# Kernel optimization log

Measured on AMD Instinct MI355X. Metric: run time of the kernel, lower is better.

## Reference

```python
import jax, jax.numpy as jnp
import numpy as np
import math

D_MODEL = 512
NUM_HEADS = 8
MAX_LEN = 10000.0


def positional_encoding_2d(seq_len, d_model, H, W, dtype=jnp.float32):
    # position along height repeated across width, and vice versa
    pos_h = jnp.repeat(jnp.arange(H, dtype=dtype), W)  # [H*W]
    pos_w = jnp.tile(jnp.arange(W, dtype=dtype), H)    # [H*W]
    div_term = jnp.exp(jnp.arange(0, d_model, 2, dtype=dtype) * (-(math.log(MAX_LEN) / d_model)))
    div = div_term[: d_model // 4]  # [d_model//4]
    pe = jnp.zeros((seq_len, d_model), dtype=dtype)
    pe = pe.at[:, 0::4].set(jnp.sin(pos_h[:, None] * div))
    pe = pe.at[:, 1::4].set(jnp.cos(pos_h[:, None] * div))
    pe = pe.at[:, 2::4].set(jnp.sin(pos_w[:, None] * div))
    pe = pe.at[:, 3::4].set(jnp.cos(pos_w[:, None] * div))
    return pe


def setup_inputs() -> dict:
    key = jax.random.key(0)
    ks = jax.random.split(key, 6)
    B, C, H, W = 8, D_MODEL, 32, 32
    d = D_MODEL
    s = 1.0 / math.sqrt(d)
    x = jax.random.normal(ks[0], (B, C, H, W), dtype=jnp.float32)
    Wq = jax.random.normal(ks[1], (d, d), dtype=jnp.float32) * s
    Wk = jax.random.normal(ks[2], (d, d), dtype=jnp.float32) * s
    Wv = jax.random.normal(ks[3], (d, d), dtype=jnp.float32) * s
    Wo = jax.random.normal(ks[4], (d, d), dtype=jnp.float32) * s
    bo = jnp.zeros((d,), dtype=jnp.float32)
    gamma = jnp.ones((d,), dtype=jnp.float32)
    beta = jnp.zeros((d,), dtype=jnp.float32)
    return {"x": x, "Wq": Wq, "Wk": Wk, "Wv": Wv, "Wo": Wo, "bo": bo, "gamma": gamma, "beta": beta}


def reference(x, Wq, Wk, Wv, Wo, bo, gamma, beta):
    B, C, H, W = x.shape
    d_model = C
    nh = NUM_HEADS
    dk = d_model // nh
    seq = H * W

    # [B, C, H, W] -> [B, seq, d_model]
    x_seq = x.reshape(B, C, seq).transpose(0, 2, 1)
    pe = positional_encoding_2d(seq, d_model, H, W, dtype=x.dtype)
    x_seq = x_seq + pe[None]
    residual = x_seq

    # QKV projections (torch Linear: y = x @ W.T)
    q = (x_seq @ Wq.T).reshape(B, seq, nh, dk).transpose(0, 2, 1, 3)  # [B, nh, S, dk]
    k = (x_seq @ Wk.T).reshape(B, seq, nh, dk).transpose(0, 2, 1, 3)
    v = (x_seq @ Wv.T).reshape(B, seq, nh, dk).transpose(0, 2, 1, 3)

    scores = jnp.einsum("bhsd,bhtd->bhst", q, k) / math.sqrt(dk)  # [B, nh, S, S]
    weights = jax.nn.softmax(scores, axis=-1)
    # dropout is identity at inference
    attn = jnp.einsum("bhst,bhtd->bhsd", weights, v)  # [B, nh, S, dk]
    attn = attn.transpose(0, 2, 1, 3).reshape(B, seq, d_model)

    out = attn @ Wo.T + bo
    y = out + residual
    mean = jnp.mean(y, axis=-1, keepdims=True)
    var = jnp.var(y, axis=-1, keepdims=True)
    y = (y - mean) / jnp.sqrt(var + 1e-5) * gamma + beta

    return y.transpose(0, 2, 1).reshape(B, C, H, W)
```

## Files before the change

kernel.cpp:

```cpp
#include <hip/hip_runtime.h>
#include <hip/hip_bf16.h>
#include <math.h>

#define DEV static __device__ __forceinline__

typedef unsigned short u16;
typedef unsigned int u32;
typedef __attribute__((ext_vector_type(4))) float f32x4;
typedef __attribute__((ext_vector_type(16))) float f32x16;
typedef __attribute__((ext_vector_type(8))) __bf16 bf16x8;
typedef __attribute__((ext_vector_type(4))) u16 u16x4;
typedef __attribute__((ext_vector_type(4))) u32 u32x4;

DEV u16 f2bf(float f) {
  unsigned u = __float_as_uint(f);
  u += 0x7fffu + ((u >> 16) & 1u);
  return (u16)(u >> 16);
}
DEV float bf2f(u16 x) { return __uint_as_float((u32)x << 16); }

DEV float fexp2(float x) { return __builtin_amdgcn_exp2f(x); }
DEV float fsin_rev(float rev) { return __builtin_amdgcn_sinf(rev); }
DEV float fcos_rev(float rev) { return __builtin_amdgcn_cosf(rev); }

DEV u32 cvt_pk_bf16(float lo, float hi) {
  u32 r;
  asm("v_cvt_pk_bf16_f32 %0, %1, %2" : "=v"(r) : "v"(lo), "v"(hi));
  return r;
}

DEV void perm32swap(u32& a, u32& b) {
  asm("v_permlane32_swap_b32 %0, %1" : "+v"(a), "+v"(b));
}

DEV void gl2lds16(const void* g, void* l) {
  __builtin_amdgcn_global_load_lds(
      (const __attribute__((address_space(1))) void*)g,
      (__attribute__((address_space(3))) void*)l, 16, 0, 0);
}

template<int RPW>
DEV void stage_rows(const u16* __restrict__ g, int gstride, u16* lds, int wave, int lane) {
  const int r_in = lane >> 3, slot = lane & 7;
  const int base_row = wave * RPW;
#pragma unroll
  for (int i = 0; i < RPW / 8; ++i) {
    const int row = base_row + i * 8 + r_in;
    const int sslot = slot ^ (row & 7);
    gl2lds16(g + (size_t)row * gstride + sslot * 8,
             lds + (size_t)(base_row + i * 8) * 64);
  }
}

DEV bf16x8 frag_read(const u16* lds, int row, int kslot) {
  const int slot = kslot ^ (row & 7);
  return *(const bf16x8*)(lds + row * 64 + slot * 8);
}

DEV f32x4 mfma16(bf16x8 a, bf16x8 b, f32x4 c) {
  return __builtin_amdgcn_mfma_f32_16x16x32_bf16(a, b, c, 0, 0, 0);
}
DEV f32x16 mfma32(bf16x8 a, bf16x8 b, f32x16 c) {
  return __builtin_amdgcn_mfma_f32_32x32x16_bf16(a, b, c, 0, 0, 0);
}

__global__ __launch_bounds__(256) void prep_x(
    const float* __restrict__ x, u16* __restrict__ Xp,
    const float* __restrict__ w0, const float* __restrict__ w1,
    const float* __restrict__ w2, const float* __restrict__ w3,
    u16* __restrict__ Wpk) {
  const int t = threadIdx.x;
  if (blockIdx.z == 8) {
    const int flat = blockIdx.x + 32 * blockIdx.y;
    const int wsel = flat >> 7, bx = flat & 127;
    const float* src = (wsel == 0) ? w0 : (wsel == 1) ? w1 : (wsel == 2) ? w2 : w3;
    const int lane = t & 63, wave = t >> 6;
    const int c16 = bx >> 2;
    const int kchunk = (bx & 3) * 4 + wave;
    const int cl = lane & 15, ko = lane >> 4;
    const float* s = src + (size_t)(c16 * 16 + cl) * 512 + kchunk * 32 + ko * 8;
    const f32x4 a = *(const f32x4*)(s);
    const f32x4 b = *(const f32x4*)(s + 4);
    u16x4 lo, hi;
#pragma unroll
    for (int j = 0; j < 4; ++j) { lo[j] = f2bf(a[j]); hi[j] = f2bf(b[j]); }
    u16* d = Wpk + (size_t)wsel * 262144
                 + (size_t)(c16 * 16 + kchunk) * 512 + lane * 8;
    *(u16x4*)(d) = lo;
    *(u16x4*)(d + 4) = hi;
    return;
  }
  __shared__ float tile[32][33];
  const int b = blockIdx.z, c0 = blockIdx.y * 32, s0 = blockIdx.x * 32;
  const int cf = t >> 5, sf = t & 31;
#pragma unroll
  for (int i = 0; i < 4; ++i) {
    const int c = c0 + cf + i * 8;
    tile[cf + i * 8][sf] = x[((size_t)b * 512 + c) * 1024 + s0 + sf];
  }
  __syncthreads();
  const int cl = t & 31, sl = t >> 5;
  const int cg = c0 + cl;
  const int j = cg >> 2;
  const float dv = fexp2((float)j * -0.051905126482615f);
  const float dv_rev = dv * 0.15915494309189535f;
#pragma unroll
  for (int i = 0; i < 4; ++i) {
    const int s = s0 + sl + i * 8;
    const float pos = (cg & 2) ? (float)(s & 31) : (float)(s >> 5);
    float rev = pos * dv_rev;
    rev = rev - floorf(rev);
    const float pe = (cg & 1) ? fcos_rev(rev) : fsin_rev(rev);
    const float v = tile[cl][sl + i * 8] + pe;
    Xp[((size_t)b * 1024 + s) * 512 + cg] = f2bf(v);
  }
}

__global__ __launch_bounds__(256) void gemm_qkv(
    const u16* __restrict__ Xp, const u16* __restrict__ Wpk,
    u16* __restrict__ Qb, u16* __restrict__ Kb, u16* __restrict__ Vtb,
    float qscale) {
  __shared__ __align__(16) u16 smem[16896];
  const int t = threadIdx.x, lane = t & 63, wave = t >> 6;
  const int bn0 = blockIdx.x * 128, bm0 = blockIdx.y * 128;
  const int wr = wave >> 1, wc = wave & 1;
  const int colbase = bn0 + wc * 64;
  const int w = colbase >> 9;
  const int cb16 = (colbase & 511) >> 4;
  const u16* Bf = Wpk + (size_t)w * 262144;
  const u16* Ag = Xp + (size_t)bm0 * 512;
  f32x4 acc[4][4] = {};
  stage_rows<32>(Ag, 512, smem, wave, lane);
  __syncthreads();
  int cur = 0;
  for (int kt = 0; kt < 512; kt += 64) {
    if (kt < 448)
      stage_rows<32>(Ag + kt + 64, 512, smem + (cur ^ 1) * 8192, wave, lane);
    u16* Asc = smem + cur * 8192;
#pragma unroll
    for (int ks = 0; ks < 2; ++ks) {
      const int kc = (kt >> 5) + ks;
      bf16x8 af[4], bfr[4];
#pragma unroll
      for (int n = 0; n < 4; ++n)
        bfr[n] = *(const bf16x8*)(Bf + (size_t)((cb16 + n) * 16 + kc) * 512 + lane * 8);
#pragma unroll
      for (int m = 0; m < 4; ++m)
        af[m] = frag_read(Asc, wr * 64 + m * 16 + (lane & 15), ks * 4 + (lane >> 4));
#pragma unroll
      for (int m = 0; m < 4; ++m)
#pragma unroll
        for (int n = 0; n < 4; ++n)
          acc[m][n] = mfma16(af[m], bfr[n], acc[m][n]);
    }
    __syncthreads();
    cur ^= 1;
  }
  const int cl = lane & 15, rg = (lane >> 4) * 4;
  if (bn0 >= 1024) {
#pragma unroll
    for (int m = 0; m < 4; ++m)
#pragma unroll
      for (int n = 0; n < 4; ++n) {
        const int dvL = wc * 64 + n * 16 + cl;
        const int rowL0 = wr * 64 + m * 16 + rg;
        u16x4 pk;
#pragma unroll
        for (int r = 0; r < 4; ++r) pk[r] = f2bf(acc[m][n][r]);
        *(u16x4*)(smem + dvL * 132 + rowL0) = pk;
      }
    __syncthreads();
    const int dvg0 = bn0 - 1024;
#pragma unroll
    for (int i = 0; i < 16; ++i) {
      const int idx = i * 256 + t;
      const int dv = idx >> 5, ch = (idx & 31) * 4;
      const u16x4 v = *(const u16x4*)(smem + dv * 132 + ch);
      *(u16x4*)(Vtb + (size_t)(dvg0 + dv) * 8192 + bm0 + ch) = v;
    }
  } else {
    u16* dst = (bn0 >= 512) ? Kb : Qb;
    const float al = (bn0 >= 512) ? 1.0f : qscale;
    const int cb = (bn0 & 511) + wc * 64;
#pragma unroll
    for (int m = 0; m < 4; ++m)
#pragma unroll
      for (int n = 0; n < 4; ++n) {
        const int col = cb + n * 16 + cl;
#pragma unroll
        for (int r = 0; r < 4; ++r) {
          const int row = bm0 + wr * 64 + m * 16 + rg + r;
          dst[(size_t)row * 512 + col] = f2bf(acc[m][n][r] * al);
        }
      }
  }
}

__global__ __launch_bounds__(512) void gemm_ln(
    const u16* __restrict__ A, const u16* __restrict__ Wpk,
    const u16* __restrict__ residb, const float* __restrict__ bias,
    const float* __restrict__ gamma, const float* __restrict__ beta,
    float* __restrict__ out) {
  __shared__ __align__(16) u16 smem[35200];
  __shared__ float redsum[8][32], redsq[8][32], srow[32][2];
  const int t = threadIdx.x, lane = t & 63, wave = t >> 6;
  const int m0 = blockIdx.x * 32;
  const int b = m0 >> 10, s0 = m0 & 1023;
  u16* As = smem;
  const u16* Bf = Wpk + (size_t)3 * 262144;
  const u16* Ag = A + (size_t)m0 * 512;
  f32x4 acc[2][4] = {};
  for (int kt = 0; kt < 512; kt += 64) {
    __syncthreads();
    if (wave < 4) stage_rows<8>(Ag + kt, 512, As, wave, lane);
    __syncthreads();
#pragma unroll
    for (int ks = 0; ks < 2; ++ks) {
      const int kc = (kt >> 5) + ks;
      bf16x8 af[2], bfr[4];
#pragma unroll
      for (int n = 0; n < 4; ++n)
        bfr[n] = *(const bf16x8*)(Bf + (size_t)((wave * 4 + n) * 16 + kc) * 512 + lane * 8);
#pragma unroll
      for (int m = 0; m < 2; ++m)
        af[m] = frag_read(As, m * 16 + (lane & 15), ks * 4 + (lane >> 4));
#pragma unroll
      for (int m = 0; m < 2; ++m)
#pragma unroll
        for (int n = 0; n < 4; ++n)
          acc[m][n] = mfma16(af[m], bfr[n], acc[m][n]);
    }
  }
  __syncthreads();
  float* fsm = (float*)smem;
  float* fw = fsm + wave * (64 * 33);
  const int cl = lane & 15, rg = (lane >> 4) * 4;
  float psum[8], psq[8];
#pragma unroll
  for (int i = 0; i < 8; ++i) { psum[i] = 0.f; psq[i] = 0.f; }
#pragma unroll
  for (int m = 0; m < 2; ++m)
#pragma unroll
    for (int n = 0; n < 4; ++n) {
      const int col_l = n * 16 + cl;
      const int col = wave * 64 + col_l;
      const float bi = bias[col];
#pragma unroll
      for (int r = 0; r < 4; ++r) {
        const int row_l = m * 16 + rg + r;
        const float v = acc[m][n][r] + bi
                      + bf2f(residb[(size_t)(m0 + row_l) * 512 + col]);
        fw[col_l * 33 + row_l] = v;
        psum[m * 4 + r] += v;
        psq[m * 4 + r] += v * v;
      }
    }
#pragma unroll
  for (int i = 0; i < 8; ++i) {
#pragma unroll
    for (int off = 8; off >= 1; off >>= 1) {
      psum[i] += __shfl_xor(psum[i], off);
      psq[i]  += __shfl_xor(psq[i], off);
    }
  }
  if (cl == 0) {
#pragma unroll
    for (int m = 0; m < 2; ++m)
#pragma unroll
      for (int r = 0; r < 4; ++r) {
        const int row_l = m * 16 + rg + r;
        redsum[wave][row_l] = psum[m * 4 + r];
        redsq[wave][row_l]  = psq[m * 4 + r];
      }
  }
  __syncthreads();
  if (t < 32) {
    float s = 0.f, q = 0.f;
#pragma unroll
    for (int w = 0; w < 8; ++w) { s += redsum[w][t]; q += redsq[w][t]; }
    const float mean = s * (1.f / 512.f);
    const float var = q * (1.f / 512.f) - mean * mean;
    srow[t][0] = mean;
    srow[t][1] = rsqrtf(var + 1e-5f);
  }
  __syncthreads();
  const int row = t & 31, cgrp = t >> 5;
  const float mean = srow[row][0], rstd = srow[row][1];
  float* outb = out + (size_t)b * 512 * 1024 + s0 + row;
#pragma unroll 4
  for (int cc = 0; cc < 32; ++cc) {
    const int col = cc * 16 + cgrp;
    const float v = (fsm[(col >> 6) * (64 * 33) + (col & 63) * 33 + row] - mean) * rstd;
    outb[(size_t)col * 1024] = v * gamma[col] + beta[col];
  }
}

__global__ __launch_bounds__(256, 4) void attn(
    const u16* __restrict__ Qb, const u16* __restrict__ Kb,
    const u16* __restrict__ Vt, u16* __restrict__ Ob) {
  __shared__ __align__(16) u16 Ks[2][64 * 64];
  __shared__ __align__(16) u16 Vs[2][64 * 64];
  const int t = threadIdx.x, lane = t & 63, wave = t >> 6;
  const int wg = blockIdx.x;
  const int b = wg & 7, h = (wg >> 3) & 7, qt = wg >> 6;
  const int qsub = wave & 1, half = wave >> 1;
  const int ql = lane & 31, hl = lane >> 5;
  const int q0 = qt * 64 + qsub * 32;
  bf16x8 bq[4];
  {
    const u16* qrow = Qb + ((size_t)b * 1024 + q0 + ql) * 512 + h * 64 + hl * 8;
#pragma unroll
    for (int c = 0; c < 4; ++c) bq[c] = *(const bf16x8*)(qrow + c * 16);
  }
  f32x16 ot[2] = {};
  float m_run = -1e30f, l_run = 0.f;
  u16* stg_dst = qsub ? Vs[half] : Ks[half];
  for (int i = 0; i < 8; ++i) {
    const int kb = half * 512 + i * 64;
    {
      const int r_in = lane >> 3, slot = lane & 7;
      const u16* src; size_t gs;
      if (qsub) { src = Vt + (size_t)(h * 64) * 8192 + (size_t)b * 1024 + kb; gs = 8192; }
      else      { src = Kb + ((size_t)b * 1024 + kb) * 512 + h * 64;          gs = 512; }
#pragma unroll
      for (int j = 0; j < 8; ++j) {
        const int row = j * 8 + r_in;
        const int ss = slot ^ (row & 7);
        gl2lds16(src + (size_t)row * gs + ss * 8, stg_dst + j * 512);
      }
    }
    __syncthreads();
    f32x16 st[2] = {};
    __builtin_amdgcn_s_setprio(1);
#pragma unroll
    for (int c = 0; c < 4; ++c) {
      bf16x8 a0 = frag_read(Ks[half], ql, c * 2 + hl);
      bf16x8 a1 = frag_read(Ks[half], 32 + ql, c * 2 + hl);
      st[0] = mfma32(a0, bq[c], st[0]);
      st[1] = mfma32(a1, bq[c], st[1]);
    }
    __builtin_amdgcn_s_setprio(0);
    float m0[8];
#pragma unroll
    for (int i2 = 0; i2 < 8; ++i2)
      m0[i2] = fmaxf(fmaxf(st[0][i2], st[0][i2 + 8]), fmaxf(st[1][i2], st[1][i2 + 8]));
#pragma unroll
    for (int i2 = 0; i2 < 4; ++i2) m0[i2] = fmaxf(m0[i2], m0[i2 + 4]);
    float mx = fmaxf(fmaxf(m0[0], m0[1]), fmaxf(m0[2], m0[3]));
    mx = fmaxf(mx, __shfl_xor(mx, 32));
    if (!__all(mx <= m_run + 8.f)) {
      const float mn = fmaxf(m_run, mx);
      const float sc = fexp2(m_run - mn);
      m_run = mn;
      l_run *= sc;
      ot[0] *= sc;
      ot[1] *= sc;
    }
#pragma unroll
    for (int i2 = 0; i2 < 16; ++i2) {
      st[0][i2] = fexp2(st[0][i2] - m_run);
      st[1][i2] = fexp2(st[1][i2] - m_run);
    }
    float s0[8];
#pragma unroll
    for (int i2 = 0; i2 < 8; ++i2)
      s0[i2] = (st[0][i2] + st[0][i2 + 8]) + (st[1][i2] + st[1][i2 + 8]);
#pragma unroll
    for (int i2 = 0; i2 < 4; ++i2) s0[i2] = s0[i2] + s0[i2 + 4];
    float rs = (s0[0] + s0[1]) + (s0[2] + s0[3]);
    rs += __shfl_xor(rs, 32);
    l_run += rs;
    __builtin_amdgcn_s_setprio(1);
#pragma unroll
    for (int c = 0; c < 4; ++c) {
      const int kf = c >> 1, i0 = (c & 1) * 4;
      u32 w0 = cvt_pk_bf16(st[kf][2 * i0 + 0], st[kf][2 * i0 + 1]);
      u32 w1 = cvt_pk_bf16(st[kf][2 * i0 + 2], st[kf][2 * i0 + 3]);
      u32 w2 = cvt_pk_bf16(st[kf][2 * i0 + 4], st[kf][2 * i0 + 5]);
      u32 w3 = cvt_pk_bf16(st[kf][2 * i0 + 6], st[kf][2 * i0 + 7]);
      perm32swap(w0, w2);
      perm32swap(w1, w3);
      u32x4 wv; wv.x = w0; wv.y = w1; wv.z = w2; wv.w = w3;
      bf16x8 bp = *(bf16x8*)&wv;
      bf16x8 v0 = frag_read(Vs[half], ql, c * 2 + hl);
      bf16x8 v1 = frag_read(Vs[half], 32 + ql, c * 2 + hl);
      ot[0] = mfma32(v0, bp, ot[0]);
      ot[1] = mfma32(v1, bp, ot[1]);
    }
    __builtin_amdgcn_s_setprio(0);
    __syncthreads();
  }
  float* Om = (float*)&Ks[0][0] + qsub * 2048;
  float* Ml = (float*)&Vs[0][0];
  if (wave >= 2) {
#pragma unroll
    for (int df = 0; df < 2; ++df)
#pragma unroll
      for (int r = 0; r < 16; ++r) {
        const int dr = (r & 3) + 8 * (r >> 2) + 4 * hl;
        Om[(df * 32 + dr) * 32 + ql] = ot[df][r];
      }
    if (hl == 0) {
      Ml[qsub * 64 + ql] = m_run;
      Ml[qsub * 64 + 32 + ql] = l_run;
    }
    __syncthreads();
  } else {
    __syncthreads();
    const float m2 = Ml[qsub * 64 + ql];
    const float l2 = Ml[qsub * 64 + 32 + ql];
    const float m = fmaxf(m_run, m2);
    const float a = fexp2(m_run - m);
    const float bsc = fexp2(m2 - m);
    const float inv = 1.f / (l_run * a + l2 * bsc);
    u16* orow = Ob + ((size_t)b * 1024 + q0 + ql) * 512 + h * 64;
#pragma unroll
    for (int df = 0; df < 2; ++df)
#pragma unroll
      for (int r = 0; r < 16; ++r) {
        const int dr = (r & 3) + 8 * (r >> 2) + 4 * hl;
        const float v = ot[df][r] * a + Om[(df * 32 + dr) * 32 + ql] * bsc;
        orow[df * 32 + dr] = f2bf(v * inv);
      }
  }
}

extern "C" void kernel_launch(void* const* d_in, const int* in_sizes, int n_in,
                              void* d_out, int out_size, void* d_ws, size_t ws_size,
                              hipStream_t stream) {
  const float* x     = (const float*)d_in[0];
  const float* Wq    = (const float*)d_in[1];
  const float* Wk    = (const float*)d_in[2];
  const float* Wv    = (const float*)d_in[3];
  const float* Wo    = (const float*)d_in[4];
  const float* bo    = (const float*)d_in[5];
  const float* gamma = (const float*)d_in[6];
  const float* beta  = (const float*)d_in[7];
  char* ws = (char*)d_ws;
  const size_t MB = 1048576;
  u16*   Xp    = (u16*)(ws);
  u16*   Wpk   = (u16*)(ws + 8 * MB);
  u16*   Qb    = (u16*)(ws + 10 * MB);
  u16*   Kb    = (u16*)(ws + 18 * MB);
  u16*   Vtb   = (u16*)(ws + 26 * MB);
  u16*   Ob    = (u16*)(ws + 34 * MB);

  prep_x<<<dim3(32, 16, 9), 256, 0, stream>>>(x, Xp, Wq, Wk, Wv, Wo, Wpk);
  gemm_qkv<<<dim3(12, 64), 256, 0, stream>>>(Xp, Wpk, Qb, Kb, Vtb,
                                             0.125f * 1.44269504088896f);
  attn<<<1024, 256, 0, stream>>>(Qb, Kb, Vtb, Ob);
  gemm_ln<<<256, 512, 0, stream>>>(Ob, Wpk, Xp, bo, gamma, beta,
                                   (float*)d_out);
}
```

Measured before the change: 80.16 us.

## Restructure attention to 2-wave blocks with double-buffered KV prefetch, drop split-K merge

The attention kernel previously used 4 waves per block, splitting the KV sequence into two halves processed by separate wave pairs, then merging partial softmax results through shared memory. Now each block has 2 waves that walk all 16 KV tiles. The next K/V tile is prefetched into the alternate buffer while the current one is computed, using explicit vmcnt waits and barriers. This removes the cross-wave merge and the load-then-wait stalls, and output stores are vectorized. In exchange there are fewer waves per block and a longer serial loop per wave.

```diff
diff --git a/kernel.cpp b/kernel.cpp
--- a/kernel.cpp
+++ b/kernel.cpp
@@ -295,7 +295,7 @@
   }
 }
 
-__global__ __launch_bounds__(256, 4) void attn(
+__global__ __launch_bounds__(128, 2) void attn(
     const u16* __restrict__ Qb, const u16* __restrict__ Kb,
     const u16* __restrict__ Vt, u16* __restrict__ Ob) {
   __shared__ __align__(16) u16 Ks[2][64 * 64];
@@ -303,9 +303,8 @@
   const int t = threadIdx.x, lane = t & 63, wave = t >> 6;
   const int wg = blockIdx.x;
   const int b = wg & 7, h = (wg >> 3) & 7, qt = wg >> 6;
-  const int qsub = wave & 1, half = wave >> 1;
   const int ql = lane & 31, hl = lane >> 5;
-  const int q0 = qt * 64 + qsub * 32;
+  const int q0 = qt * 64 + wave * 32;
   bf16x8 bq[4];
   {
     const u16* qrow = Qb + ((size_t)b * 1024 + q0 + ql) * 512 + h * 64 + hl * 8;
@@ -314,28 +313,52 @@
   }
   f32x16 ot[2] = {};
   float m_run = -1e30f, l_run = 0.f;
-  u16* stg_dst = qsub ? Vs[half] : Ks[half];
-  for (int i = 0; i < 8; ++i) {
-    const int kb = half * 512 + i * 64;
-    {
-      const int r_in = lane >> 3, slot = lane & 7;
-      const u16* src; size_t gs;
-      if (qsub) { src = Vt + (size_t)(h * 64) * 8192 + (size_t)b * 1024 + kb; gs = 8192; }
-      else      { src = Kb + ((size_t)b * 1024 + kb) * 512 + h * 64;          gs = 512; }
-#pragma unroll
-      for (int j = 0; j < 8; ++j) {
-        const int row = j * 8 + r_in;
-        const int ss = slot ^ (row & 7);
-        gl2lds16(src + (size_t)row * gs + ss * 8, stg_dst + j * 512);
-      }
-    }
-    __syncthreads();
+  const u16* Kg = Kb + (size_t)b * 1024 * 512 + h * 64;
+  const u16* Vg = Vt + (size_t)(h * 64) * 8192 + (size_t)b * 1024;
+  const int r_in = lane >> 3, slot = lane & 7;
+#define STAGE_TILE(kv, buf)                                                   \
+  do {                                                                        \
+    if (wave == 0) {                                                          \
+      const u16* src = Kg + (size_t)(kv) * 64 * 512;                          \
+      _Pragma("unroll")                                                       \
+      for (int j = 0; j < 8; ++j) {                                           \
+        const int row = j * 8 + r_in;                                         \
+        const int ss = slot ^ (row & 7);                                      \
+        gl2lds16(src + (size_t)row * 512 + ss * 8, &Ks[buf][j * 512]);        \
+      }                                                                       \
+    } else {                                                                  \
+      const u16* src = Vg + (kv) * 64;                                        \
+      _Pragma("unroll")                                                       \
+      for (int j = 0; j < 8; ++j) {                                           \
+        const int row = j * 8 + r_in;                                         \
+        const int ss = slot ^ (row & 7);                                      \
+        gl2lds16(src + (size_t)row * 8192 + ss * 8, &Vs[buf][j * 512]);       \
+      }                                                                       \
+    }                                                                         \
+  } while (0)
+
+  STAGE_TILE(0, 0);
+  __builtin_amdgcn_sched_barrier(0);
+  asm volatile("s_waitcnt vmcnt(0)" ::: "memory");
+  __builtin_amdgcn_s_barrier();
+  __builtin_amdgcn_sched_barrier(0);
+  int cur = 0;
+  for (int kv = 0; kv < 16; ++kv) {
+    if (kv < 15) {
+      STAGE_TILE(kv + 1, cur ^ 1);
+      __builtin_amdgcn_sched_barrier(0);
+      asm volatile("s_waitcnt vmcnt(8)" ::: "memory");
+    } else {
+      asm volatile("s_waitcnt vmcnt(0)" ::: "memory");
+    }
+    __builtin_amdgcn_s_barrier();
+    __builtin_amdgcn_sched_barrier(0);
     f32x16 st[2] = {};
     __builtin_amdgcn_s_setprio(1);
 #pragma unroll
     for (int c = 0; c < 4; ++c) {
-      bf16x8 a0 = frag_read(Ks[half], ql, c * 2 + hl);
-      bf16x8 a1 = frag_read(Ks[half], 32 + ql, c * 2 + hl);
+      bf16x8 a0 = frag_read(Ks[cur], ql, c * 2 + hl);
+      bf16x8 a1 = frag_read(Ks[cur], 32 + ql, c * 2 + hl);
       st[0] = mfma32(a0, bq[c], st[0]);
       st[1] = mfma32(a1, bq[c], st[1]);
     }
@@ -382,47 +405,29 @@
       perm32swap(w1, w3);
       u32x4 wv; wv.x = w0; wv.y = w1; wv.z = w2; wv.w = w3;
       bf16x8 bp = *(bf16x8*)&wv;
-      bf16x8 v0 = frag_read(Vs[half], ql, c * 2 + hl);
-      bf16x8 v1 = frag_read(Vs[half], 32 + ql, c * 2 + hl);
+      bf16x8 v0 = frag_read(Vs[cur], ql, c * 2 + hl);
+      bf16x8 v1 = frag_read(Vs[cur], 32 + ql, c * 2 + hl);
       ot[0] = mfma32(v0, bp, ot[0]);
       ot[1] = mfma32(v1, bp, ot[1]);
     }
     __builtin_amdgcn_s_setprio(0);
-    __syncthreads();
-  }
-  float* Om = (float*)&Ks[0][0] + qsub * 2048;
-  float* Ml = (float*)&Vs[0][0];
-  if (wave >= 2) {
-#pragma unroll
-    for (int df = 0; df < 2; ++df)
-#pragma unroll
-      for (int r = 0; r < 16; ++r) {
-        const int dr = (r & 3) + 8 * (r >> 2) + 4 * hl;
-        Om[(df * 32 + dr) * 32 + ql] = ot[df][r];
-      }
-    if (hl == 0) {
-      Ml[qsub * 64 + ql] = m_run;
-      Ml[qsub * 64 + 32 + ql] = l_run;
-    }
-    __syncthreads();
-  } else {
-    __syncthreads();
-    const float m2 = Ml[qsub * 64 + ql];
-    const float l2 = Ml[qsub * 64 + 32 + ql];
-    const float m = fmaxf(m_run, m2);
-    const float a = fexp2(m_run - m);
-    const float bsc = fexp2(m2 - m);
-    const float inv = 1.f / (l_run * a + l2 * bsc);
-    u16* orow = Ob + ((size_t)b * 1024 + q0 + ql) * 512 + h * 64;
-#pragma unroll
-    for (int df = 0; df < 2; ++df)
-#pragma unroll
-      for (int r = 0; r < 16; ++r) {
-        const int dr = (r & 3) + 8 * (r >> 2) + 4 * hl;
-        const float v = ot[df][r] * a + Om[(df * 32 + dr) * 32 + ql] * bsc;
-        orow[df * 32 + dr] = f2bf(v * inv);
-      }
-  }
+    __builtin_amdgcn_sched_barrier(0);
+    __builtin_amdgcn_s_barrier();
+    __builtin_amdgcn_sched_barrier(0);
+    cur ^= 1;
+  }
+#undef STAGE_TILE
+  const float inv = 1.f / l_run;
+  u16* orow = Ob + ((size_t)b * 1024 + q0 + ql) * 512 + h * 64;
+#pragma unroll
+  for (int df = 0; df < 2; ++df)
+#pragma unroll
+    for (int rq = 0; rq < 4; ++rq) {
+      u16x4 pk;
+#pragma unroll
+      for (int j = 0; j < 4; ++j) pk[j] = f2bf(ot[df][rq * 4 + j] * inv);
+      *(u16x4*)(orow + df * 32 + rq * 8 + 4 * hl) = pk;
+    }
 }
 
 extern "C" void kernel_launch(void* const* d_in, const int* in_sizes, int n_in,
@@ -448,7 +453,7 @@
   prep_x<<<dim3(32, 16, 9), 256, 0, stream>>>(x, Xp, Wq, Wk, Wv, Wo, Wpk);
   gemm_qkv<<<dim3(12, 64), 256, 0, stream>>>(Xp, Wpk, Qb, Kb, Vtb,
                                              0.125f * 1.44269504088896f);
-  attn<<<1024, 256, 0, stream>>>(Qb, Kb, Vtb, Ob);
+  attn<<<1024, 128, 0, stream>>>(Qb, Kb, Vtb, Ob);
   gemm_ln<<<256, 512, 0, stream>>>(Ob, Wpk, Xp, bo, gamma, beta,
                                    (float*)d_out);
 }
```

Measured after the change: 81.65 us. About the same (+1.9%).
